# Optimization experiments

Hardware: AMD Instinct MI355X
Metric: run time of the kernel (lower is better)

## Reference

```python
import jax, jax.numpy as jnp
import numpy as np

NUM_BUSES = 96
HPB = 64            # hidden neurons per bus
INPUT_SIZE = 2048
FPB = 21            # input features per bus (96*21 + 9 global = 2025 <= 2048)
OPB = 21            # output targets per bus
NUM_HIDDEN_LAYERS = 4
HIDDEN = NUM_BUSES * HPB      # 6144
OUT = NUM_BUSES * OPB         # 2016
BATCH = 4096
NEG_SLOPE = 0.01


def _build_masks():
    # input -> first hidden: each bus block sees its own features + 9 global cols
    m0 = np.zeros((HIDDEN, INPUT_SIZE), np.float32)
    for b in range(NUM_BUSES):
        m0[b * HPB:(b + 1) * HPB, b * FPB:(b + 1) * FPB] = 1.0
    m0[:, INPUT_SIZE - 9:] = 1.0
    # hidden -> hidden: ring graph, neighbors {b-1, b, b+1}
    mh = np.zeros((HIDDEN, HIDDEN), np.float32)
    for b in range(NUM_BUSES):
        for n in ((b - 1) % NUM_BUSES, b, (b + 1) % NUM_BUSES):
            mh[n * HPB:(n + 1) * HPB, b * HPB:(b + 1) * HPB] = 1.0
    # last hidden -> output: bus b's targets see only bus b's hidden block
    mo = np.zeros((OUT, HIDDEN), np.float32)
    for b in range(NUM_BUSES):
        mo[b * OPB:(b + 1) * OPB, b * HPB:(b + 1) * HPB] = 1.0
    return jnp.asarray(m0), jnp.asarray(mh), jnp.asarray(mo)


def setup_inputs() -> dict:
    key = jax.random.key(0)
    ks = jax.random.split(key, 11)
    M0, Mh, Mo = _build_masks()
    s_in = 1.0 / np.sqrt(INPUT_SIZE)
    s_h = 1.0 / np.sqrt(HIDDEN)
    return {
        "x": jax.random.normal(ks[0], (BATCH, INPUT_SIZE), jnp.float32),
        "W0": jax.random.normal(ks[1], (HIDDEN, INPUT_SIZE), jnp.float32) * s_in,
        "b0": jax.random.normal(ks[2], (HIDDEN,), jnp.float32) * s_in,
        "W1": jax.random.normal(ks[3], (HIDDEN, HIDDEN), jnp.float32) * s_h,
        "b1": jax.random.normal(ks[4], (HIDDEN,), jnp.float32) * s_h,
        "W2": jax.random.normal(ks[5], (HIDDEN, HIDDEN), jnp.float32) * s_h,
        "b2": jax.random.normal(ks[6], (HIDDEN,), jnp.float32) * s_h,
        "W3": jax.random.normal(ks[7], (HIDDEN, HIDDEN), jnp.float32) * s_h,
        "b3": jax.random.normal(ks[8], (HIDDEN,), jnp.float32) * s_h,
        "Wo": jax.random.normal(ks[9], (OUT, HIDDEN), jnp.float32) * s_h,
        "bo": jax.random.normal(ks[10], (OUT,), jnp.float32) * s_h,
        "M0": M0, "M1": Mh, "M2": Mh, "M3": Mh, "Mo": Mo,
    }


def _leaky(v):
    return jnp.where(v >= 0, v, NEG_SLOPE * v)


def reference(x, W0, b0, W1, b1, W2, b2, W3, b3, Wo, bo, M0, M1, M2, M3, Mo):
    # PAWNNLayer: y = x @ (W * mask).T + b ; LeakyReLU between all layers except last
    h = _leaky(x @ (W0 * M0).T + b0)
    h = _leaky(h @ (W1 * M1).T + b1)
    h = _leaky(h @ (W2 * M2).T + b2)
    h = _leaky(h @ (W3 * M3).T + b3)
    return h @ (Wo * Mo).T + bo
```

## Files before the change

### kernel.cpp

```cpp
#include <hip/hip_runtime.h>

#define NB    96
#define HID   6144
#define INSZ  2048
#define FPB   21
#define OPB   21
#define OUTD  2016
#define BATCH 4096
#define NEG   0.01f

typedef _Float16 half8 __attribute__((ext_vector_type(8)));
typedef float floatx4 __attribute__((ext_vector_type(4)));

__device__ __forceinline__ unsigned short f2h_bits(float f) {
    union { _Float16 h; unsigned short u; } v;
    v.h = (_Float16)f;
    return v.u;
}

__global__ __launch_bounds__(256) void pack_weights(
    const float* __restrict__ W0, const float* __restrict__ W1,
    const float* __restrict__ W2, const float* __restrict__ W3,
    const float* __restrict__ Wo,
    unsigned short* __restrict__ whpF,
    unsigned short* __restrict__ w0F,
    unsigned short* __restrict__ woF)
{
    const int NH = 3 * NB * 12288;
    const int N0 = NB * 2048;
    const int NO = NB * 2048;
    int idx = blockIdx.x * 256 + threadIdx.x;
    if (idx < NH) {
        int e = idx;
        int l = e / 1179648;
        int r = e - l * 1179648;
        int bus = r / 12288;
        int r1 = r - bus * 12288;
        int kk = r1 >> 11;
        int r2 = r1 & 2047;
        int u = r2 >> 9;
        int r3 = r2 & 511;
        int lane = r3 >> 3, j = r3 & 7;
        int mq = lane & 15, q = lane >> 4;
        int col = u * 16 + mq;
        int k = kk * 32 + q * 8 + j;
        int src_b = (bus + 95 + (k >> 6)) % NB;
        const float* W = (l == 0) ? W1 : (l == 1) ? W2 : W3;
        float v = W[(size_t)(bus * 64 + col) * HID + src_b * 64 + (k & 63)];
        whpF[e] = f2h_bits(v);
    } else if (idx < NH + N0) {
        int e = idx - NH;
        int bus = e >> 11;
        int r = e & 2047;
        int u = r >> 9;
        int r2 = r & 511;
        int lane = r2 >> 3, j = r2 & 7;
        int mq = lane & 15, q = lane >> 4;
        int col = u * 16 + mq;
        int k = q * 8 + j;
        float v = 0.f;
        if (k < FPB)      v = W0[(size_t)(bus * 64 + col) * INSZ + bus * FPB + k];
        else if (k < 30)  v = W0[(size_t)(bus * 64 + col) * INSZ + (INSZ - 9) + (k - FPB)];
        w0F[e] = f2h_bits(v);
    } else if (idx < NH + N0 + NO) {
        int e = idx - NH - N0;
        int bus = e >> 11;
        int r = e & 2047;
        int kk = r >> 10;
        int r2 = r & 1023;
        int u = r2 >> 9;
        int r3 = r2 & 511;
        int lane = r3 >> 3, j = r3 & 7;
        int mq = lane & 15, q = lane >> 4;
        int row32 = u * 16 + mq;
        int k = kk * 32 + q * 8 + j;
        float v = 0.f;
        if (row32 < OPB)
            v = Wo[(size_t)(bus * OPB + row32) * HID + bus * 64 + k];
        woF[e] = f2h_bits(v);
    }
}

__device__ __forceinline__ void mid_prefetch(
    const unsigned short* __restrict__ hin, unsigned short* AsBuf,
    int tid, int gbase_row, int cb0, int cb1, int cb2)
{
    #pragma unroll
    for (int i = 0; i < 6; ++i) {
        int g = i * 256 + tid;
        int row = g / 24;
        int j = g - row * 24;
        int kg = j - (row % 24);
        kg += (kg < 0) ? 24 : 0;
        const unsigned short* src = hin + (size_t)(gbase_row + row) * HID
                                  + (kg < 8 ? cb0 : (kg < 16 ? cb1 : cb2)) + (kg & 7) * 8;
        __builtin_amdgcn_global_load_lds(
            (const __attribute__((address_space(1))) unsigned int*)src,
            (__attribute__((address_space(3))) unsigned int*)(AsBuf + (size_t)(i * 256 + (tid & ~63)) * 8),
            16, 0, 0);
    }
}

__global__ __launch_bounds__(256) void mid_kernel(
    const unsigned short* __restrict__ hin,
    const unsigned short* __restrict__ WpF,
    const float* __restrict__ bias,
    unsigned short* __restrict__ hout)
{
    __shared__ unsigned short AsF[2][1536 * 8];
    const int lin = blockIdx.y * NB + blockIdx.x;
    const int xcd = lin & 7;
    const int idx = lin >> 3;
    const int bus = xcd * 12 + (idx % 12);
    const int rowblk = (idx / 12) * 256;
    const int tid = threadIdx.x;
    const int lane = tid & 63, wid = tid >> 6;
    const int mq = lane & 15, q = lane >> 4;
    const int cb0 = ((bus + 95) % NB) * 64;
    const int cb1 = bus * 64;
    const int cb2 = ((bus + 1) % NB) * 64;

    half8 bfr[6][4];
    #pragma unroll
    for (int kk = 0; kk < 6; ++kk)
        #pragma unroll
        for (int u = 0; u < 4; ++u)
            bfr[kk][u] = *(const half8*)(WpF + (size_t)(((bus * 6 + kk) * 4 + u) * 512) + lane * 8);

    float bv[4];
    #pragma unroll
    for (int u = 0; u < 4; ++u) bv[u] = bias[bus * 64 + u * 16 + mq];

    mid_prefetch(hin, &AsF[0][0], tid, rowblk, cb0, cb1, cb2);
    __syncthreads();

    const int row = wid * 16 + mq;
    const int r24 = row % 24;
    const int qr = q + r24;

    for (int c = 0; c < 4; ++c) {
        int buf = c & 1;
        if (c < 3)
            mid_prefetch(hin, &AsF[buf ^ 1][0], tid, rowblk + (c + 1) * 64, cb0, cb1, cb2);

        floatx4 acc[4];
        #pragma unroll
        for (int u = 0; u < 4; ++u) acc[u] = (floatx4){0.f, 0.f, 0.f, 0.f};

        #pragma unroll
        for (int kk = 0; kk < 6; ++kk) {
            int vv = 4 * kk + qr;
            if (vv >= 24) vv -= 24;
            half8 a = *(const half8*)(&AsF[buf][(row * 24 + vv) * 8]);
            #pragma unroll
            for (int u = 0; u < 4; ++u)
                acc[u] = __builtin_amdgcn_mfma_f32_16x16x32_f16(a, bfr[kk][u], acc[u], 0, 0, 0);
        }

        int orow = rowblk + c * 64 + wid * 16 + q * 4;
        #pragma unroll
        for (int u = 0; u < 4; ++u) {
            int colg = bus * 64 + u * 16 + mq;
            #pragma unroll
            for (int r = 0; r < 4; ++r) {
                float v = acc[u][r] + bv[u];
                v = (v >= 0.f) ? v : NEG * v;
                hout[(size_t)(orow + r) * HID + colg] = f2h_bits(v);
            }
        }
        __syncthreads();
    }
}

__global__ __launch_bounds__(256) void layer0_kernel(
    const float* __restrict__ x,
    const unsigned short* __restrict__ w0F,
    const float* __restrict__ b0,
    unsigned short* __restrict__ hout)
{
    __shared__ unsigned short As[128][40];
    int bus = blockIdx.x, rb = blockIdx.y * 128, tid = threadIdx.x;
    int lane = tid & 63, wid = tid >> 6, mq = lane & 15, q = lane >> 4;

    half8 b0f[4];
    #pragma unroll
    for (int u = 0; u < 4; ++u)
        b0f[u] = *(const half8*)(w0F + (size_t)(bus * 4 + u) * 512 + lane * 8);

    #pragma unroll
    for (int i = 0; i < 16; ++i) {
        int g = i * 256 + tid;
        int row = g >> 5, k = g & 31;
        float v = 0.f;
        if (k < FPB)      v = x[(size_t)(rb + row) * INSZ + bus * FPB + k];
        else if (k < 30)  v = x[(size_t)(rb + row) * INSZ + (INSZ - 9) + (k - FPB)];
        As[row][k] = f2h_bits(v);
    }
    __syncthreads();

    int m_base = wid * 32;
    floatx4 acc[2][4];
    #pragma unroll
    for (int t = 0; t < 2; ++t)
        #pragma unroll
        for (int u = 0; u < 4; ++u)
            acc[t][u] = (floatx4){0.f, 0.f, 0.f, 0.f};

    half8 a0 = *(const half8*)(&As[m_base + mq][q * 8]);
    half8 a1 = *(const half8*)(&As[m_base + 16 + mq][q * 8]);
    #pragma unroll
    for (int u = 0; u < 4; ++u) {
        acc[0][u] = __builtin_amdgcn_mfma_f32_16x16x32_f16(a0, b0f[u], acc[0][u], 0, 0, 0);
        acc[1][u] = __builtin_amdgcn_mfma_f32_16x16x32_f16(a1, b0f[u], acc[1][u], 0, 0, 0);
    }

    #pragma unroll
    for (int t = 0; t < 2; ++t)
        #pragma unroll
        for (int u = 0; u < 4; ++u) {
            int col = bus * 64 + u * 16 + mq;
            float bvv = b0[col];
            #pragma unroll
            for (int r = 0; r < 4; ++r) {
                int rowg = rb + m_base + t * 16 + q * 4 + r;
                float v = acc[t][u][r] + bvv;
                v = (v >= 0.f) ? v : NEG * v;
                hout[(size_t)rowg * HID + col] = f2h_bits(v);
            }
        }
}

__global__ __launch_bounds__(256) void out_kernel(
    const unsigned short* __restrict__ hin,
    const unsigned short* __restrict__ woF,
    const float* __restrict__ bo,
    float* __restrict__ out)
{
    __shared__ unsigned short As[128][72];
    int bus = blockIdx.x, rb = blockIdx.y * 128, tid = threadIdx.x;
    int lane = tid & 63, wid = tid >> 6, mq = lane & 15, q = lane >> 4;

    half8 wf[2][2];
    #pragma unroll
    for (int kk = 0; kk < 2; ++kk)
        #pragma unroll
        for (int u = 0; u < 2; ++u)
            wf[kk][u] = *(const half8*)(woF + (size_t)(((bus * 2 + kk) * 2 + u) * 512) + lane * 8);

    #pragma unroll
    for (int i = 0; i < 4; ++i) {
        int g = i * 256 + tid;
        int row = g >> 3, kg = g & 7;
        *(uint4*)(&As[row][kg * 8]) =
            *(const uint4*)(hin + (size_t)(rb + row) * HID + bus * 64 + kg * 8);
    }
    __syncthreads();

    int m_base = wid * 32;
    floatx4 acc[2][2];
    #pragma unroll
    for (int t = 0; t < 2; ++t)
        #pragma unroll
        for (int u = 0; u < 2; ++u)
            acc[t][u] = (floatx4){0.f, 0.f, 0.f, 0.f};

    #pragma unroll
    for (int kk = 0; kk < 2; ++kk) {
        int ko = kk * 32 + q * 8;
        half8 a0 = *(const half8*)(&As[m_base + mq][ko]);
        half8 a1 = *(const half8*)(&As[m_base + 16 + mq][ko]);
        #pragma unroll
        for (int u = 0; u < 2; ++u) {
            acc[0][u] = __builtin_amdgcn_mfma_f32_16x16x32_f16(a0, wf[kk][u], acc[0][u], 0, 0, 0);
            acc[1][u] = __builtin_amdgcn_mfma_f32_16x16x32_f16(a1, wf[kk][u], acc[1][u], 0, 0, 0);
        }
    }

    #pragma unroll
    for (int t = 0; t < 2; ++t)
        #pragma unroll
        for (int u = 0; u < 2; ++u) {
            int c32 = u * 16 + mq;
            if (c32 < OPB) {
                float bvv = bo[bus * OPB + c32];
                #pragma unroll
                for (int r = 0; r < 4; ++r) {
                    int rowg = rb + m_base + t * 16 + q * 4 + r;
                    out[(size_t)rowg * OUTD + bus * OPB + c32] = acc[t][u][r] + bvv;
                }
            }
        }
}

extern "C" void kernel_launch(void* const* d_in, const int* in_sizes, int n_in,
                              void* d_out, int out_size, void* d_ws, size_t ws_size,
                              hipStream_t stream) {
    const float* x  = (const float*)d_in[0];
    const float* W0 = (const float*)d_in[1];
    const float* b0 = (const float*)d_in[2];
    const float* W1 = (const float*)d_in[3];
    const float* b1 = (const float*)d_in[4];
    const float* W2 = (const float*)d_in[5];
    const float* b2 = (const float*)d_in[6];
    const float* W3 = (const float*)d_in[7];
    const float* b3 = (const float*)d_in[8];
    const float* Wo = (const float*)d_in[9];
    const float* bo = (const float*)d_in[10];
    float* out = (float*)d_out;

    char* ws = (char*)d_ws;
    unsigned short* whpF = (unsigned short*)(ws);
    unsigned short* w0F  = (unsigned short*)(ws + 7077888);
    unsigned short* woF  = (unsigned short*)(ws + 7471104);
    unsigned short* hA   = (unsigned short*)(ws + 7864320);
    unsigned short* hB   = (unsigned short*)(ws + 58195968);

    const int PACK_TOTAL = 3 * NB * 12288 + NB * 2048 + NB * 2048;
    pack_weights<<<dim3(PACK_TOTAL / 256), dim3(256), 0, stream>>>(
        W0, W1, W2, W3, Wo, whpF, w0F, woF);

    layer0_kernel<<<dim3(NB, 32), dim3(256), 0, stream>>>(x, w0F, b0, hA);
    mid_kernel<<<dim3(NB, 16), dim3(256), 0, stream>>>(hA, whpF,               b1, hB);
    mid_kernel<<<dim3(NB, 16), dim3(256), 0, stream>>>(hB, whpF + 1179648,     b2, hA);
    mid_kernel<<<dim3(NB, 16), dim3(256), 0, stream>>>(hA, whpF + 2 * 1179648, b3, hB);
    out_kernel<<<dim3(NB, 32), dim3(256), 0, stream>>>(hB, woF, bo, out);
}
```

Before: 794.7 us.

## Fuse last hidden layer with output projection and use fine-grained vmcnt waits

Merges the third hidden-layer kernel with the output layer, so the per-bus hidden block goes through shared memory straight into the output MFMA instead of being written to global memory and read back. This removes one launch and a full fp16 activation round trip. It also swaps the full __syncthreads in the mid-layer loop for explicit s_waitcnt vmcnt counts plus s_barrier, so the next chunk's prefetch can stay in flight while the current chunk computes. The hand-coded vmcnt counts depend on the exact number of loads the compiler emits, and the scratch tile reuses the current LDS buffer, which adds correctness risk.

```diff
diff --git a/kernel.cpp b/kernel.cpp
--- a/kernel.cpp
+++ b/kernel.cpp
@@ -132,16 +132,21 @@
     for (int u = 0; u < 4; ++u) bv[u] = bias[bus * 64 + u * 16 + mq];
 
     mid_prefetch(hin, &AsF[0][0], tid, rowblk, cb0, cb1, cb2);
-    __syncthreads();
 
     const int row = wid * 16 + mq;
     const int r24 = row % 24;
     const int qr = q + r24;
 
+    #pragma unroll
     for (int c = 0; c < 4; ++c) {
         int buf = c & 1;
         if (c < 3)
             mid_prefetch(hin, &AsF[buf ^ 1][0], tid, rowblk + (c + 1) * 64, cb0, cb1, cb2);
+
+        if (c == 0)      asm volatile("s_waitcnt vmcnt(6)"  ::: "memory");
+        else if (c == 3) asm volatile("s_waitcnt vmcnt(16)" ::: "memory");
+        else             asm volatile("s_waitcnt vmcnt(22)" ::: "memory");
+        __builtin_amdgcn_s_barrier();
 
         floatx4 acc[4];
         #pragma unroll
@@ -168,7 +173,122 @@
                 hout[(size_t)(orow + r) * HID + colg] = f2h_bits(v);
             }
         }
-        __syncthreads();
+        if (c < 3) __builtin_amdgcn_s_barrier();
+    }
+}
+
+__global__ __launch_bounds__(256) void mid_out_kernel(
+    const unsigned short* __restrict__ hin,
+    const unsigned short* __restrict__ WpF,
+    const float* __restrict__ bias,
+    const unsigned short* __restrict__ woF,
+    const float* __restrict__ bo,
+    float* __restrict__ out)
+{
+    __shared__ unsigned short AsF[2][1536 * 8];
+    const int lin = blockIdx.y * NB + blockIdx.x;
+    const int xcd = lin & 7;
+    const int idx = lin >> 3;
+    const int bus = xcd * 12 + (idx % 12);
+    const int rowblk = (idx / 12) * 256;
+    const int tid = threadIdx.x;
+    const int lane = tid & 63, wid = tid >> 6;
+    const int mq = lane & 15, q = lane >> 4;
+    const int cb0 = ((bus + 95) % NB) * 64;
+    const int cb1 = bus * 64;
+    const int cb2 = ((bus + 1) % NB) * 64;
+
+    half8 bfr[6][4];
+    #pragma unroll
+    for (int kk = 0; kk < 6; ++kk)
+        #pragma unroll
+        for (int u = 0; u < 4; ++u)
+            bfr[kk][u] = *(const half8*)(WpF + (size_t)(((bus * 6 + kk) * 4 + u) * 512) + lane * 8);
+
+    half8 wf[2][2];
+    #pragma unroll
+    for (int kk = 0; kk < 2; ++kk)
+        #pragma unroll
+        for (int u = 0; u < 2; ++u)
+            wf[kk][u] = *(const half8*)(woF + (size_t)(((bus * 2 + kk) * 2 + u) * 512) + lane * 8);
+
+    float bv[4];
+    #pragma unroll
+    for (int u = 0; u < 4; ++u) bv[u] = bias[bus * 64 + u * 16 + mq];
+
+    float bvo[2];
+    #pragma unroll
+    for (int u = 0; u < 2; ++u) {
+        int c32 = u * 16 + mq;
+        bvo[u] = (c32 < OPB) ? bo[bus * OPB + c32] : 0.f;
+    }
+
+    mid_prefetch(hin, &AsF[0][0], tid, rowblk, cb0, cb1, cb2);
+
+    const int row = wid * 16 + mq;
+    const int r24 = row % 24;
+    const int qr = q + r24;
+
+    #pragma unroll
+    for (int c = 0; c < 4; ++c) {
+        int buf = c & 1;
+        if (c < 3)
+            mid_prefetch(hin, &AsF[buf ^ 1][0], tid, rowblk + (c + 1) * 64, cb0, cb1, cb2);
+
+        if (c == 0)      asm volatile("s_waitcnt vmcnt(6)"  ::: "memory");
+        else if (c == 3) asm volatile("s_waitcnt vmcnt(8)"  ::: "memory");
+        else             asm volatile("s_waitcnt vmcnt(14)" ::: "memory");
+        __builtin_amdgcn_s_barrier();
+
+        floatx4 acc[4];
+        #pragma unroll
+        for (int u = 0; u < 4; ++u) acc[u] = (floatx4){0.f, 0.f, 0.f, 0.f};
+
+        #pragma unroll
+        for (int kk = 0; kk < 6; ++kk) {
+            int vv = 4 * kk + qr;
+            if (vv >= 24) vv -= 24;
+            half8 a = *(const half8*)(&AsF[buf][(row * 24 + vv) * 8]);
+            #pragma unroll
+            for (int u = 0; u < 4; ++u)
+                acc[u] = __builtin_amdgcn_mfma_f32_16x16x32_f16(a, bfr[kk][u], acc[u], 0, 0, 0);
+        }
+
+        unsigned short* myscr = &AsF[buf][wid * 3072];
+        #pragma unroll
+        for (int u = 0; u < 4; ++u) {
+            #pragma unroll
+            for (int r = 0; r < 4; ++r) {
+                float v = acc[u][r] + bv[u];
+                v = (v >= 0.f) ? v : NEG * v;
+                myscr[(q * 4 + r) * 80 + u * 16 + mq] = f2h_bits(v);
+            }
+        }
+
+        floatx4 acco[2];
+        #pragma unroll
+        for (int u = 0; u < 2; ++u) acco[u] = (floatx4){0.f, 0.f, 0.f, 0.f};
+
+        #pragma unroll
+        for (int kk = 0; kk < 2; ++kk) {
+            half8 a = *(const half8*)(myscr + mq * 80 + kk * 32 + q * 8);
+            #pragma unroll
+            for (int u = 0; u < 2; ++u)
+                acco[u] = __builtin_amdgcn_mfma_f32_16x16x32_f16(a, wf[kk][u], acco[u], 0, 0, 0);
+        }
+
+        int orow = rowblk + c * 64 + wid * 16 + q * 4;
+        #pragma unroll
+        for (int u = 0; u < 2; ++u) {
+            int c32 = u * 16 + mq;
+            if (c32 < OPB) {
+                #pragma unroll
+                for (int r = 0; r < 4; ++r)
+                    out[(size_t)(orow + r) * OUTD + bus * OPB + c32] = acco[u][r] + bvo[u];
+            }
+        }
+
+        if (c < 3) __builtin_amdgcn_s_barrier();
     }
 }
 
@@ -226,68 +346,6 @@
                 float v = acc[t][u][r] + bvv;
                 v = (v >= 0.f) ? v : NEG * v;
                 hout[(size_t)rowg * HID + col] = f2h_bits(v);
-            }
-        }
-}
-
-__global__ __launch_bounds__(256) void out_kernel(
-    const unsigned short* __restrict__ hin,
-    const unsigned short* __restrict__ woF,
-    const float* __restrict__ bo,
-    float* __restrict__ out)
-{
-    __shared__ unsigned short As[128][72];
-    int bus = blockIdx.x, rb = blockIdx.y * 128, tid = threadIdx.x;
-    int lane = tid & 63, wid = tid >> 6, mq = lane & 15, q = lane >> 4;
-
-    half8 wf[2][2];
-    #pragma unroll
-    for (int kk = 0; kk < 2; ++kk)
-        #pragma unroll
-        for (int u = 0; u < 2; ++u)
-            wf[kk][u] = *(const half8*)(woF + (size_t)(((bus * 2 + kk) * 2 + u) * 512) + lane * 8);
-
-    #pragma unroll
-    for (int i = 0; i < 4; ++i) {
-        int g = i * 256 + tid;
-        int row = g >> 3, kg = g & 7;
-        *(uint4*)(&As[row][kg * 8]) =
-            *(const uint4*)(hin + (size_t)(rb + row) * HID + bus * 64 + kg * 8);
-    }
-    __syncthreads();
-
-    int m_base = wid * 32;
-    floatx4 acc[2][2];
-    #pragma unroll
-    for (int t = 0; t < 2; ++t)
-        #pragma unroll
-        for (int u = 0; u < 2; ++u)
-            acc[t][u] = (floatx4){0.f, 0.f, 0.f, 0.f};
-
-    #pragma unroll
-    for (int kk = 0; kk < 2; ++kk) {
-        int ko = kk * 32 + q * 8;
-        half8 a0 = *(const half8*)(&As[m_base + mq][ko]);
-        half8 a1 = *(const half8*)(&As[m_base + 16 + mq][ko]);
-        #pragma unroll
-        for (int u = 0; u < 2; ++u) {
-            acc[0][u] = __builtin_amdgcn_mfma_f32_16x16x32_f16(a0, wf[kk][u], acc[0][u], 0, 0, 0);
-            acc[1][u] = __builtin_amdgcn_mfma_f32_16x16x32_f16(a1, wf[kk][u], acc[1][u], 0, 0, 0);
-        }
-    }
-
-    #pragma unroll
-    for (int t = 0; t < 2; ++t)
-        #pragma unroll
-        for (int u = 0; u < 2; ++u) {
-            int c32 = u * 16 + mq;
-            if (c32 < OPB) {
-                float bvv = bo[bus * OPB + c32];
-                #pragma unroll
-                for (int r = 0; r < 4; ++r) {
-                    int rowg = rb + m_base + t * 16 + q * 4 + r;
-                    out[(size_t)rowg * OUTD + bus * OPB + c32] = acc[t][u][r] + bvv;
-                }
             }
         }
 }
@@ -320,8 +378,8 @@
         W0, W1, W2, W3, Wo, whpF, w0F, woF);
 
     layer0_kernel<<<dim3(NB, 32), dim3(256), 0, stream>>>(x, w0F, b0, hA);
-    mid_kernel<<<dim3(NB, 16), dim3(256), 0, stream>>>(hA, whpF,               b1, hB);
-    mid_kernel<<<dim3(NB, 16), dim3(256), 0, stream>>>(hB, whpF + 1179648,     b2, hA);
-    mid_kernel<<<dim3(NB, 16), dim3(256), 0, stream>>>(hA, whpF + 2 * 1179648, b3, hB);
-    out_kernel<<<dim3(NB, 32), dim3(256), 0, stream>>>(hB, woF, bo, out);
-}
+    mid_kernel<<<dim3(NB, 16), dim3(256), 0, stream>>>(hA, whpF,           b1, hB);
+    mid_kernel<<<dim3(NB, 16), dim3(256), 0, stream>>>(hB, whpF + 1179648, b2, hA);
+    mid_out_kernel<<<dim3(NB, 16), dim3(256), 0, stream>>>(
+        hA, whpF + 2 * 1179648, b3, woF, bo, out);
+}
```

After: 775.2 us. 1.03x faster.
